# Optimization experiments

Hardware: AMD Instinct MI355X
Metric: run time of the kernel (lower is better)

Reference implementation:

```python
import jax, jax.numpy as jnp
import numpy as np

HIDDEN_DIM = 1024
HEAD_DIM = 64


def setup_inputs() -> dict:
    key = jax.random.key(0)
    kx, kq, kk, kv, ko = jax.random.split(key, 5)
    B, S = 4, 4096
    x = jax.random.normal(kx, (B, S, HIDDEN_DIM), dtype=jnp.float32)
    # nn.Linear(in, out, bias=False) weight has shape [out, in]; y = x @ W.T
    scale = 1.0 / np.sqrt(HIDDEN_DIM)
    Wq = jax.random.normal(kq, (HEAD_DIM, HIDDEN_DIM), dtype=jnp.float32) * scale
    Wk = jax.random.normal(kk, (HEAD_DIM, HIDDEN_DIM), dtype=jnp.float32) * scale
    Wv = jax.random.normal(kv, (HEAD_DIM, HIDDEN_DIM), dtype=jnp.float32) * scale
    Wo = jax.random.normal(ko, (HIDDEN_DIM, HEAD_DIM), dtype=jnp.float32) * (1.0 / np.sqrt(HEAD_DIM))
    return {"x": x, "Wq": Wq, "Wk": Wk, "Wv": Wv, "Wo": Wo}


def reference(x, Wq, Wk, Wv, Wo):
    # projections: x [B,S,H] @ W.T [H,D] -> [B,S,D]
    q = jnp.einsum('bsh,dh->bsd', x, Wq)
    k = jnp.einsum('bsh,dh->bsd', x, Wk)
    v = jnp.einsum('bsh,dh->bsd', x, Wv)
    d = q.shape[-1]
    scores = jnp.einsum('bqd,bkd->bqk', q, k) / jnp.sqrt(jnp.asarray(d, q.dtype))
    S = q.shape[1]
    causal_mask = jnp.triu(jnp.ones((S, S), dtype=bool), k=1)  # True above diagonal
    scores = jnp.where(causal_mask[None, :, :], jnp.asarray(-jnp.inf, scores.dtype), scores)
    attn = jax.nn.softmax(scores, axis=-1)
    out = jnp.einsum('bqk,bkd->bqd', attn, v)
    return jnp.einsum('bsd,hd->bsh', out, Wo)
```

## Files before the change

### kernel.cpp

```cpp
#include <hip/hip_runtime.h>
#include <hip/hip_bf16.h>


typedef __attribute__((ext_vector_type(8))) __bf16 bf16x8;
typedef __attribute__((ext_vector_type(4))) float f32x4;

#define BATCH 4
#define SEQ   4096
#define HID   1024
#define HDIM  64
#define CHT   8
#define NCMAX 8

__device__ __forceinline__ unsigned short f2bf(float f) {
  unsigned u = __builtin_bit_cast(unsigned, f);
  u += 0x7fffu + ((u >> 16) & 1u);
  return (unsigned short)(u >> 16);
}
__device__ __forceinline__ float bf2f(unsigned short u) {
  unsigned v = ((unsigned)u) << 16;
  return __builtin_bit_cast(float, v);
}
__device__ __forceinline__ __bf16 f2bf16(float f) {
  unsigned short us = f2bf(f);
  return __builtin_bit_cast(__bf16, us);
}
__device__ __forceinline__ bf16x8 pack8(f32x4 a, f32x4 b) {
  bf16x8 r;
  r[0] = f2bf16(a[0]); r[1] = f2bf16(a[1]); r[2] = f2bf16(a[2]); r[3] = f2bf16(a[3]);
  r[4] = f2bf16(b[0]); r[5] = f2bf16(b[1]); r[6] = f2bf16(b[2]); r[7] = f2bf16(b[3]);
  return r;
}

__global__ __launch_bounds__(256) void convert_w(
    const float* __restrict__ Wq, const float* __restrict__ Wk,
    const float* __restrict__ Wv, const float* __restrict__ Wo,
    unsigned short* __restrict__ q, unsigned short* __restrict__ k,
    unsigned short* __restrict__ v, unsigned short* __restrict__ o) {
  const int gid = blockIdx.x * 256 + threadIdx.x;
  const int mat = gid >> 16, idx = gid & 0xFFFF;
  const float* s = (mat == 0) ? Wq : (mat == 1) ? Wk : (mat == 2) ? Wv : Wo;
  unsigned short* d = (mat == 0) ? q : (mat == 1) ? k : (mat == 2) ? v : o;
  d[idx] = f2bf(s[idx]);
}

__global__ __launch_bounds__(64) void qkv_proj(
    const float* __restrict__ x,
    const unsigned short* __restrict__ Wqb,
    const unsigned short* __restrict__ Wkb,
    const unsigned short* __restrict__ Wvb,
    unsigned short* __restrict__ Q,
    unsigned short* __restrict__ K,
    unsigned short* __restrict__ Vt) {
  const int mb   = blockIdx.x;
  const int lane = threadIdx.x;
  const int quad = lane >> 4;
  const int l15  = lane & 15;
  const int row0 = mb * 16;

  const unsigned short* Ws[3] = {Wqb, Wkb, Wvb};

  f32x4 acc[3][4];
  const f32x4 zero = {0.f, 0.f, 0.f, 0.f};
#pragma unroll
  for (int z = 0; z < 3; ++z)
#pragma unroll
    for (int n = 0; n < 4; ++n) acc[z][n] = zero;

  const float* ap = x + (size_t)(row0 + l15) * HID + quad * 8;

  f32x4 af[2][2];
  af[0][0] = *reinterpret_cast<const f32x4*>(ap);
  af[0][1] = *reinterpret_cast<const f32x4*>(ap + 4);
  af[1][0] = *reinterpret_cast<const f32x4*>(ap + 32);
  af[1][1] = *reinterpret_cast<const f32x4*>(ap + 36);

  int slot = 0;
  for (int kk = 0; kk < HID; kk += 32) {
    bf16x8 a = pack8(af[slot][0], af[slot][1]);
    if (kk + 64 < HID) {
      af[slot][0] = *reinterpret_cast<const f32x4*>(ap + kk + 64);
      af[slot][1] = *reinterpret_cast<const f32x4*>(ap + kk + 68);
    }
    slot ^= 1;
#pragma unroll
    for (int z = 0; z < 3; ++z)
#pragma unroll
      for (int n = 0; n < 4; ++n) {
        bf16x8 b = *reinterpret_cast<const bf16x8*>(Ws[z] + (size_t)(n * 16 + l15) * HID + kk + quad * 8);
        acc[z][n] = __builtin_amdgcn_mfma_f32_16x16x32_bf16(a, b, acc[z][n], 0, 0, 0);
      }
  }

#pragma unroll
  for (int z = 0; z < 2; ++z) {
    unsigned short* Out = (z == 0) ? Q : K;
#pragma unroll
    for (int n = 0; n < 4; ++n)
#pragma unroll
      for (int r = 0; r < 4; ++r) {
        const int row = row0 + quad * 4 + r;
        const int col = n * 16 + l15;
        Out[(size_t)row * HDIM + col] = f2bf(acc[z][n][r]);
      }
  }
#pragma unroll
  for (int n = 0; n < 4; ++n)
#pragma unroll
    for (int r = 0; r < 4; ++r) {
      const int row = row0 + quad * 4 + r;
      const int col = n * 16 + l15;
      const int bb = row >> 12, sl = row & 4095;
      Vt[(size_t)bb * HDIM * SEQ + (size_t)col * SEQ + sl] = f2bf(acc[2][n][r]);
    }
}

#define LSTR 72

__global__ __launch_bounds__(256) void flash_splitk(
    const unsigned short* __restrict__ Qg,
    const unsigned short* __restrict__ Kg,
    const unsigned short* __restrict__ Vt,
    unsigned short* __restrict__ Og,
    unsigned short* __restrict__ Opart,
    float2* __restrict__ Ml) {
  const int qb = blockIdx.x;
  const int b  = blockIdx.y;
  const int c  = blockIdx.z;
  const int nc = (qb >> 3) + 1;
  if (c >= nc) return;
  const int j0 = c * CHT;
  const int j1 = min(j0 + CHT, qb + 1);

  const int tid  = threadIdx.x;
  const int lane = tid & 63;
  const int wave = tid >> 6;
  const int quad = lane >> 4;
  const int l15  = lane & 15;

  __shared__ unsigned short kt[64 * LSTR];
  __shared__ unsigned short vt[64 * LSTR];
  __shared__ unsigned short pt[4][16 * LSTR];

  const size_t base  = (size_t)b * SEQ * HDIM;
  const size_t baseT = (size_t)b * HDIM * SEQ;
  const int qrow0 = qb * 64 + wave * 16;

  bf16x8 aq[2];
  {
    const unsigned short* qp = Qg + base + (size_t)(qrow0 + l15) * HDIM + quad * 8;
    aq[0] = *reinterpret_cast<const bf16x8*>(qp);
    aq[1] = *reinterpret_cast<const bf16x8*>(qp + 32);
  }

  f32x4 o[4];
  const f32x4 zero = {0.f, 0.f, 0.f, 0.f};
#pragma unroll
  for (int n = 0; n < 4; ++n) o[n] = zero;
  float m_i[4], l_i[4];
#pragma unroll
  for (int r = 0; r < 4; ++r) { m_i[r] = -__builtin_inff(); l_i[r] = 0.f; }

  unsigned short* pw = pt[wave];
  const int srow = tid >> 2, sc0 = (tid & 3) * 16;
  const unsigned short* kb = Kg + base;
  const unsigned short* vb = Vt + baseT;

  const float C = 0.125f * 1.44269504f;

  uint4 pk0, pk1, pv0, pv1;
  {
    const uint4* kp = reinterpret_cast<const uint4*>(kb + (size_t)(j0 * 64 + srow) * HDIM + sc0);
    pk0 = kp[0]; pk1 = kp[1];
    const uint4* vp = reinterpret_cast<const uint4*>(vb + (size_t)srow * SEQ + j0 * 64 + sc0);
    pv0 = vp[0]; pv1 = vp[1];
    *reinterpret_cast<uint4*>(&kt[srow * LSTR + sc0])     = pk0;
    *reinterpret_cast<uint4*>(&kt[srow * LSTR + sc0 + 8]) = pk1;
    *reinterpret_cast<uint4*>(&vt[srow * LSTR + sc0])     = pv0;
    *reinterpret_cast<uint4*>(&vt[srow * LSTR + sc0 + 8]) = pv1;
  }

  for (int j = j0; j < j1; ++j) {
    __syncthreads();
    const bool pre = (j + 1 < j1);
    if (pre) {
      const uint4* kp = reinterpret_cast<const uint4*>(kb + (size_t)((j + 1) * 64 + srow) * HDIM + sc0);
      pk0 = kp[0]; pk1 = kp[1];
      const uint4* vp = reinterpret_cast<const uint4*>(vb + (size_t)srow * SEQ + (j + 1) * 64 + sc0);
      pv0 = vp[0]; pv1 = vp[1];
    }

    f32x4 s[4];
#pragma unroll
    for (int n = 0; n < 4; ++n) s[n] = zero;
#pragma unroll
    for (int ks = 0; ks < 2; ++ks) {
#pragma unroll
      for (int n = 0; n < 4; ++n) {
        bf16x8 bk = *reinterpret_cast<const bf16x8*>(&kt[(n * 16 + l15) * LSTR + ks * 32 + quad * 8]);
        s[n] = __builtin_amdgcn_mfma_f32_16x16x32_bf16(aq[ks], bk, s[n], 0, 0, 0);
      }
    }

    if (j == qb) {
#pragma unroll
      for (int n = 0; n < 4; ++n) {
        const int col = n * 16 + l15;
#pragma unroll
        for (int r = 0; r < 4; ++r) {
          const int rowl = wave * 16 + quad * 4 + r;
          if (col > rowl) s[n][r] = -__builtin_inff();
        }
      }
    }

    float mnew[4], alpha[4], mC[4];
#pragma unroll
    for (int r = 0; r < 4; ++r) {
      float v = fmaxf(fmaxf(s[0][r], s[1][r]), fmaxf(s[2][r], s[3][r]));
#pragma unroll
      for (int off = 1; off < 16; off <<= 1) v = fmaxf(v, __shfl_xor(v, off, 64));
      mnew[r]  = fmaxf(m_i[r], v);
      alpha[r] = __builtin_amdgcn_exp2f((m_i[r] - mnew[r]) * C);
      mC[r]    = mnew[r] * C;
    }
    float p[4][4];
#pragma unroll
    for (int n = 0; n < 4; ++n)
#pragma unroll
      for (int r = 0; r < 4; ++r)
        p[n][r] = __builtin_amdgcn_exp2f(__builtin_fmaf(s[n][r], C, -mC[r]));
#pragma unroll
    for (int r = 0; r < 4; ++r) {
      float v = (p[0][r] + p[1][r]) + (p[2][r] + p[3][r]);
#pragma unroll
      for (int off = 1; off < 16; off <<= 1) v += __shfl_xor(v, off, 64);
      l_i[r] = l_i[r] * alpha[r] + v;
      m_i[r] = mnew[r];
    }
#pragma unroll
    for (int n = 0; n < 4; ++n)
#pragma unroll
      for (int r = 0; r < 4; ++r) o[n][r] *= alpha[r];

#pragma unroll
    for (int n = 0; n < 4; ++n)
#pragma unroll
      for (int r = 0; r < 4; ++r)
        pw[(quad * 4 + r) * LSTR + n * 16 + l15] = f2bf(p[n][r]);

#pragma unroll
    for (int ks = 0; ks < 2; ++ks) {
      bf16x8 ap = *reinterpret_cast<const bf16x8*>(&pw[l15 * LSTR + ks * 32 + quad * 8]);
#pragma unroll
      for (int n = 0; n < 4; ++n) {
        bf16x8 bv = *reinterpret_cast<const bf16x8*>(&vt[(n * 16 + l15) * LSTR + ks * 32 + quad * 8]);
        o[n] = __builtin_amdgcn_mfma_f32_16x16x32_bf16(ap, bv, o[n], 0, 0, 0);
      }
    }

    __syncthreads();
    if (pre) {
      *reinterpret_cast<uint4*>(&kt[srow * LSTR + sc0])     = pk0;
      *reinterpret_cast<uint4*>(&kt[srow * LSTR + sc0 + 8]) = pk1;
      *reinterpret_cast<uint4*>(&vt[srow * LSTR + sc0])     = pv0;
      *reinterpret_cast<uint4*>(&vt[srow * LSTR + sc0 + 8]) = pv1;
    }
  }

  if (nc == 1) {
#pragma unroll
    for (int n = 0; n < 4; ++n)
#pragma unroll
      for (int r = 0; r < 4; ++r) {
        const int row = qrow0 + quad * 4 + r;
        const int col = n * 16 + l15;
        Og[base + (size_t)row * HDIM + col] = f2bf(o[n][r] / l_i[r]);
      }
  } else {
    const int slot = ((b * 64 + qb) << 3) + c;
#pragma unroll
    for (int n = 0; n < 4; ++n)
#pragma unroll
      for (int r = 0; r < 4; ++r) {
        const int rowl = wave * 16 + quad * 4 + r;
        const int col  = n * 16 + l15;
        Opart[(size_t)slot * 4096 + rowl * 64 + col] = f2bf(o[n][r]);
      }
    if (l15 == 0) {
#pragma unroll
      for (int r = 0; r < 4; ++r) {
        const int rowl = wave * 16 + quad * 4 + r;
        Ml[slot * 64 + rowl] = make_float2(m_i[r], l_i[r]);
      }
    }
  }
}

__global__ __launch_bounds__(256) void merge_splitk(
    const unsigned short* __restrict__ Opart,
    const float2* __restrict__ Ml,
    unsigned short* __restrict__ Og) {
  const int qb = blockIdx.x;
  if (qb < CHT) return;
  const int b  = blockIdx.y;
  const int nc = (qb >> 3) + 1;
  const int row = threadIdx.x >> 2;
  const int cg  = (threadIdx.x & 3) * 16;
  const int slot0 = (b * 64 + qb) << 3;

  float m[NCMAX], l[NCMAX];
  float M = -__builtin_inff();
  for (int c = 0; c < nc; ++c) {
    float2 ml = Ml[(slot0 + c) * 64 + row];
    m[c] = ml.x; l[c] = ml.y;
    M = fmaxf(M, m[c]);
  }
  const float C = 0.125f * 1.44269504f;
  float L = 0.f, acc[16];
#pragma unroll
  for (int i = 0; i < 16; ++i) acc[i] = 0.f;
  for (int c = 0; c < nc; ++c) {
    const float w = __builtin_amdgcn_exp2f((m[c] - M) * C);
    L += w * l[c];
    const unsigned short* p = Opart + (size_t)(slot0 + c) * 4096 + row * 64 + cg;
    uint4 u0 = *reinterpret_cast<const uint4*>(p);
    uint4 u1 = *reinterpret_cast<const uint4*>(p + 8);
    const unsigned* uu = &u0.x;
#pragma unroll
    for (int i = 0; i < 4; ++i) {
      acc[2 * i]     += w * bf2f((unsigned short)(uu[i] & 0xFFFF));
      acc[2 * i + 1] += w * bf2f((unsigned short)(uu[i] >> 16));
    }
    const unsigned* vv = &u1.x;
#pragma unroll
    for (int i = 0; i < 4; ++i) {
      acc[8 + 2 * i]     += w * bf2f((unsigned short)(vv[i] & 0xFFFF));
      acc[8 + 2 * i + 1] += w * bf2f((unsigned short)(vv[i] >> 16));
    }
  }
  const float inv = 1.f / L;
  uint4 o0, o1;
  unsigned* po = &o0.x;
#pragma unroll
  for (int i = 0; i < 4; ++i)
    po[i] = (unsigned)f2bf(acc[2 * i] * inv) | ((unsigned)f2bf(acc[2 * i + 1] * inv) << 16);
  unsigned* p1 = &o1.x;
#pragma unroll
  for (int i = 0; i < 4; ++i)
    p1[i] = (unsigned)f2bf(acc[8 + 2 * i] * inv) | ((unsigned)f2bf(acc[8 + 2 * i + 1] * inv) << 16);
  unsigned short* dst = Og + (size_t)b * SEQ * HDIM + (size_t)(qb * 64 + row) * HDIM + cg;
  *reinterpret_cast<uint4*>(dst)     = o0;
  *reinterpret_cast<uint4*>(dst + 8) = o1;
}

__global__ __launch_bounds__(256) void out_proj(
    const unsigned short* __restrict__ O,
    const unsigned short* __restrict__ Wob,
    float* __restrict__ Y) {
  const int nb   = blockIdx.x;
  const int mb   = blockIdx.y;
  const int lane = threadIdx.x & 63;
  const int wave = threadIdx.x >> 6;
  const int quad = lane >> 4;
  const int l15  = lane & 15;
  const int row0 = mb * 64 + wave * 16;

  f32x4 acc[4];
  const f32x4 zero = {0.f, 0.f, 0.f, 0.f};
#pragma unroll
  for (int n = 0; n < 4; ++n) acc[n] = zero;

  const unsigned short* op = O + (size_t)(row0 + l15) * HDIM + quad * 8;
  bf16x8 a0 = *reinterpret_cast<const bf16x8*>(op);
  bf16x8 a1 = *reinterpret_cast<const bf16x8*>(op + 32);
#pragma unroll
  for (int n = 0; n < 4; ++n) {
    const int col = nb * 64 + n * 16 + l15;
    const unsigned short* wp = Wob + (size_t)col * HDIM + quad * 8;
    bf16x8 b0 = *reinterpret_cast<const bf16x8*>(wp);
    bf16x8 b1 = *reinterpret_cast<const bf16x8*>(wp + 32);
    acc[n] = __builtin_amdgcn_mfma_f32_16x16x32_bf16(a0, b0, acc[n], 0, 0, 0);
    acc[n] = __builtin_amdgcn_mfma_f32_16x16x32_bf16(a1, b1, acc[n], 0, 0, 0);
  }
#pragma unroll
  for (int n = 0; n < 4; ++n)
#pragma unroll
    for (int r = 0; r < 4; ++r) {
      const int row = row0 + quad * 4 + r;
      const int col = nb * 64 + n * 16 + l15;
      Y[(size_t)row * HID + col] = acc[n][r];
    }
}

extern "C" void kernel_launch(void* const* d_in, const int* in_sizes, int n_in,
                              void* d_out, int out_size, void* d_ws, size_t ws_size,
                              hipStream_t stream) {
  const float* x  = (const float*)d_in[0];
  const float* Wq = (const float*)d_in[1];
  const float* Wk = (const float*)d_in[2];
  const float* Wv = (const float*)d_in[3];
  const float* Wo = (const float*)d_in[4];
  float* Y = (float*)d_out;

  const size_t qkv_elems = (size_t)BATCH * SEQ * HDIM;
  const size_t w_elems   = (size_t)HDIM * HID;
  unsigned short* Q     = (unsigned short*)d_ws;
  unsigned short* K     = Q + qkv_elems;
  unsigned short* Vt    = K + qkv_elems;
  unsigned short* O     = Vt + qkv_elems;
  unsigned short* Wqb   = O + qkv_elems;
  unsigned short* Wkb   = Wqb + w_elems;
  unsigned short* Wvb   = Wkb + w_elems;
  unsigned short* Wob   = Wvb + w_elems;
  unsigned short* Opart = Wob + w_elems;
  float2*         Ml    = (float2*)(Opart + (size_t)2048 * 4096);

  convert_w   <<<1024,               256, 0, stream>>>(Wq, Wk, Wv, Wo, Wqb, Wkb, Wvb, Wob);
  qkv_proj    <<<1024,                64, 0, stream>>>(x, Wqb, Wkb, Wvb, Q, K, Vt);
  flash_splitk<<<dim3(64, 4, NCMAX), 256, 0, stream>>>(Q, K, Vt, O, Opart, Ml);
  merge_splitk<<<dim3(64, 4),        256, 0, stream>>>(Opart, Ml, O);
  out_proj    <<<dim3(16, 256),      256, 0, stream>>>(O, Wob, Y);
}
```

Before: 244.2 us.

## Stage x tiles in LDS via async global_load_lds and split QKV projection across four waves

The QKV projection kernel now uses 256-thread blocks covering 32 rows. Each pair of waves shares a 16-row x tile, and each wave computes half of the 64 output columns. Tiles of x are streamed into double-buffered, XOR-swizzled shared memory with direct global-to-LDS loads instead of per-lane register prefetch. The aim is to raise memory-level parallelism and occupancy and to halve per-wave weight traffic per row tile, at the cost of a block barrier every k-step and half as many blocks.

```diff
diff --git a/kernel.cpp b/kernel.cpp
--- a/kernel.cpp
+++ b/kernel.cpp
@@ -44,7 +44,7 @@
   d[idx] = f2bf(s[idx]);
 }
 
-__global__ __launch_bounds__(64) void qkv_proj(
+__global__ __launch_bounds__(256) void qkv_proj(
     const float* __restrict__ x,
     const unsigned short* __restrict__ Wqb,
     const unsigned short* __restrict__ Wkb,
@@ -53,42 +53,58 @@
     unsigned short* __restrict__ K,
     unsigned short* __restrict__ Vt) {
   const int mb   = blockIdx.x;
-  const int lane = threadIdx.x;
+  const int tid  = threadIdx.x;
+  const int lane = tid & 63;
+  const int wave = tid >> 6;
   const int quad = lane >> 4;
   const int l15  = lane & 15;
-  const int row0 = mb * 16;
+  const int rt   = wave >> 1;
+  const int nh   = wave & 1;
+  const int ar   = rt * 16 + l15;
+  const int row0 = mb * 32 + rt * 16;
+
+  __shared__ float xs[2][32 * 32];
 
   const unsigned short* Ws[3] = {Wqb, Wkb, Wvb};
 
-  f32x4 acc[3][4];
+  f32x4 acc[3][2];
   const f32x4 zero = {0.f, 0.f, 0.f, 0.f};
 #pragma unroll
   for (int z = 0; z < 3; ++z)
 #pragma unroll
-    for (int n = 0; n < 4; ++n) acc[z][n] = zero;
-
-  const float* ap = x + (size_t)(row0 + l15) * HID + quad * 8;
-
-  f32x4 af[2][2];
-  af[0][0] = *reinterpret_cast<const f32x4*>(ap);
-  af[0][1] = *reinterpret_cast<const f32x4*>(ap + 4);
-  af[1][0] = *reinterpret_cast<const f32x4*>(ap + 32);
-  af[1][1] = *reinterpret_cast<const f32x4*>(ap + 36);
-
-  int slot = 0;
+    for (int n2 = 0; n2 < 2; ++n2) acc[z][n2] = zero;
+
+  const int srow   = tid >> 3;
+  const int schunk = (tid & 7) ^ (srow & 7);
+  const float* sgp = x + (size_t)(mb * 32 + srow) * HID + schunk * 4;
+  float* lb0 = &xs[0][wave * 256];
+  float* lb1 = &xs[1][wave * 256];
+
+  const int ra0 = ar * 32 + ((2 * quad)     ^ (ar & 7)) * 4;
+  const int ra1 = ar * 32 + ((2 * quad + 1) ^ (ar & 7)) * 4;
+
+  __builtin_amdgcn_global_load_lds(
+      (const __attribute__((address_space(1))) void*)sgp,
+      (__attribute__((address_space(3))) void*)lb0, 16, 0, 0);
+
   for (int kk = 0; kk < HID; kk += 32) {
-    bf16x8 a = pack8(af[slot][0], af[slot][1]);
-    if (kk + 64 < HID) {
-      af[slot][0] = *reinterpret_cast<const f32x4*>(ap + kk + 64);
-      af[slot][1] = *reinterpret_cast<const f32x4*>(ap + kk + 68);
-    }
-    slot ^= 1;
+    const int buf = (kk >> 5) & 1;
+    __syncthreads();
+    if (kk + 32 < HID) {
+      __builtin_amdgcn_global_load_lds(
+          (const __attribute__((address_space(1))) void*)(sgp + kk + 32),
+          (__attribute__((address_space(3))) void*)(buf ? lb0 : lb1), 16, 0, 0);
+    }
+    f32x4 alo = *reinterpret_cast<const f32x4*>(&xs[buf][ra0]);
+    f32x4 ahi = *reinterpret_cast<const f32x4*>(&xs[buf][ra1]);
+    bf16x8 a = pack8(alo, ahi);
 #pragma unroll
     for (int z = 0; z < 3; ++z)
 #pragma unroll
-      for (int n = 0; n < 4; ++n) {
-        bf16x8 b = *reinterpret_cast<const bf16x8*>(Ws[z] + (size_t)(n * 16 + l15) * HID + kk + quad * 8);
-        acc[z][n] = __builtin_amdgcn_mfma_f32_16x16x32_bf16(a, b, acc[z][n], 0, 0, 0);
+      for (int n2 = 0; n2 < 2; ++n2) {
+        const int col = nh * 32 + n2 * 16 + l15;
+        bf16x8 b = *reinterpret_cast<const bf16x8*>(Ws[z] + (size_t)col * HID + kk + quad * 8);
+        acc[z][n2] = __builtin_amdgcn_mfma_f32_16x16x32_bf16(a, b, acc[z][n2], 0, 0, 0);
       }
   }
 
@@ -96,22 +112,22 @@
   for (int z = 0; z < 2; ++z) {
     unsigned short* Out = (z == 0) ? Q : K;
 #pragma unroll
-    for (int n = 0; n < 4; ++n)
+    for (int n2 = 0; n2 < 2; ++n2)
 #pragma unroll
       for (int r = 0; r < 4; ++r) {
         const int row = row0 + quad * 4 + r;
-        const int col = n * 16 + l15;
-        Out[(size_t)row * HDIM + col] = f2bf(acc[z][n][r]);
-      }
-  }
-#pragma unroll
-  for (int n = 0; n < 4; ++n)
+        const int col = nh * 32 + n2 * 16 + l15;
+        Out[(size_t)row * HDIM + col] = f2bf(acc[z][n2][r]);
+      }
+  }
+#pragma unroll
+  for (int n2 = 0; n2 < 2; ++n2)
 #pragma unroll
     for (int r = 0; r < 4; ++r) {
       const int row = row0 + quad * 4 + r;
-      const int col = n * 16 + l15;
+      const int col = nh * 32 + n2 * 16 + l15;
       const int bb = row >> 12, sl = row & 4095;
-      Vt[(size_t)bb * HDIM * SEQ + (size_t)col * SEQ + sl] = f2bf(acc[2][n][r]);
+      Vt[(size_t)bb * HDIM * SEQ + (size_t)col * SEQ + sl] = f2bf(acc[2][n2][r]);
     }
 }
 
@@ -417,7 +433,7 @@
   float2*         Ml    = (float2*)(Opart + (size_t)2048 * 4096);
 
   convert_w   <<<1024,               256, 0, stream>>>(Wq, Wk, Wv, Wo, Wqb, Wkb, Wvb, Wob);
-  qkv_proj    <<<1024,                64, 0, stream>>>(x, Wqb, Wkb, Wvb, Q, K, Vt);
+  qkv_proj    <<<512,                256, 0, stream>>>(x, Wqb, Wkb, Wvb, Q, K, Vt);
   flash_splitk<<<dim3(64, 4, NCMAX), 256, 0, stream>>>(Q, K, Vt, O, Opart, Ml);
   merge_splitk<<<dim3(64, 4),        256, 0, stream>>>(Opart, Ml, O);
   out_proj    <<<dim3(16, 256),      256, 0, stream>>>(O, Wob, Y);
```

After: 239.2 us. 1.02x faster.
